# Optimization experiments

Measured on AMD Instinct MI355X. Metric: run time of the kernel, lower is better.

The kernel has to match this reference:

```python
import jax, jax.numpy as jnp
import numpy as np

RES = (64, 128, 256, 512)
CH = (4, 4, 4, 4)          # hidden_dim_voxel
N = 1 << 20                # query points
IN = sum(CH)               # MLP input dim = 16
WIDTH = 64
DEPTH = 4
OUT = 4
A = -0.75                  # torch bicubic coefficient


def setup_inputs() -> dict:
    key = jax.random.key(0)
    ks = jax.random.split(key, 16)
    inp = {"x": jax.random.normal(ks[0], (N, 2), jnp.float32)}
    for i, (r, c) in enumerate(zip(RES, CH)):
        # torch.rand init for voxel data, stored as [C, H, W]
        inp[f"data{i}"] = jax.random.uniform(ks[1 + i], (c, r, r), dtype=jnp.float32)
    dims = [IN] + [WIDTH] * DEPTH
    for i in range(DEPTH):
        fan = dims[i]
        inp[f"w{i}"] = jax.random.normal(ks[5 + i], (fan, WIDTH), jnp.float32) / np.sqrt(fan)
        inp[f"b{i}"] = jnp.zeros((WIDTH,), jnp.float32)
    inp["wout"] = jax.random.normal(ks[9], (WIDTH, OUT), jnp.float32) / np.sqrt(WIDTH)
    inp["bout"] = jnp.zeros((OUT,), jnp.float32)
    return inp


def _cc1(t):  # |x| in [0,1]
    return ((A + 2.0) * t - (A + 3.0)) * t * t + 1.0


def _cc2(t):  # |x| in (1,2]
    return ((A * t - 5.0 * A) * t + 8.0 * A) * t - 4.0 * A


def _cubic_w(t):
    # weights for taps at offsets (-1, 0, 1, 2); t is fractional part, shape [N]
    return jnp.stack([_cc2(t + 1.0), _cc1(t), _cc1(1.0 - t), _cc2(2.0 - t)])  # [4, N]


def _grid_sample_bicubic(data, iy, ix):
    # data: [C, H, W]; iy/ix: unnormalized (align_corners=True) coords, [N]
    # padding_mode='border' -> clamp tap indices
    C, H, W = data.shape
    x0 = jnp.floor(ix)
    y0 = jnp.floor(iy)
    tx = ix - x0
    ty = iy - y0
    offs = jnp.arange(-1, 3, dtype=jnp.int32)[:, None]          # [4,1]
    xs = jnp.clip(x0.astype(jnp.int32)[None] + offs, 0, W - 1)  # [4,N]
    ys = jnp.clip(y0.astype(jnp.int32)[None] + offs, 0, H - 1)  # [4,N]
    wx = _cubic_w(tx)  # [4,N]
    wy = _cubic_w(ty)  # [4,N]
    patch = data[:, ys[:, None, :], xs[None, :, :]]             # [C,4,4,N]
    return jnp.einsum('cijn,in,jn->nc', patch, wy, wx)          # [N,C]


def _forward(x, datas, ws, bs, wout, bout):
    s = jax.nn.sigmoid(x)  # input_activation, enable_act=True
    # Voxel: g = s*2-1, flip(-1); grid_sample align_corners=True unnormalize:
    # (g+1)/2*(size-1) == s*(size-1). After flip, grid x (width) = s[:,1], y = s[:,0].
    feats = []
    for data in datas:
        H = data.shape[1]
        iy = s[:, 0] * (H - 1)
        ix = s[:, 1] * (H - 1)
        feats.append(_grid_sample_bicubic(data, iy, ix))
    h = jnp.concatenate(feats, axis=-1)  # [N, 16]
    inputs = h  # MLP called with enable_act=False
    for i, (w, b) in enumerate(zip(ws, bs)):
        h = jax.nn.relu(h @ w + b)
        if i % 4 == 0 and i > 0:  # skip_layer=4; never triggers for depth=4
            h = jnp.concatenate([h, inputs], axis=-1)
    return h @ wout + bout  # [N, OUT]


def reference(x, data0, data1, data2, data3, w0, b0, w1, b1, w2, b2, w3, b3, wout, bout):
    return _forward(x, (data0, data1, data2, data3), (w0, w1, w2, w3), (b0, b1, b2, b3), wout, bout)
```

## Files before the change

kernel.cpp:

```cpp
#include <hip/hip_runtime.h>

#define A_COEF (-0.75f)

typedef unsigned int u32;
using f16x8 = __attribute__((ext_vector_type(8))) _Float16;
using f32x16 = __attribute__((ext_vector_type(16))) float;

#define NBINS 4096
#define HB    128
#define NBLK  1024

#define ILV_TOTAL  1392640
#define ILV_BLOCKS 5440
#define FRG_BLOCKS 8
#define PREP_BLOCKS (ILV_BLOCKS + FRG_BLOCKS + HB)

__device__ __forceinline__ float cc1(float t) {
    return ((A_COEF + 2.0f) * t - (A_COEF + 3.0f)) * t * t + 1.0f;
}
__device__ __forceinline__ float cc2(float t) {
    return ((A_COEF * t - 5.0f * A_COEF) * t + 8.0f * A_COEF) * t - 4.0f * A_COEF;
}

__device__ __forceinline__ u32 pkrtz(float a, float b) {
    u32 r;
    asm("v_cvt_pkrtz_f16_f32 %0, %1, %2" : "=v"(r) : "v"(a), "v"(b));
    return r;
}

__device__ __forceinline__ int point_bin(float2 xv) {
    float sy = 1.0f / (1.0f + __expf(-xv.x));
    float sx = 1.0f / (1.0f + __expf(-xv.y));
    int qy = min(63, (int)(sy * 64.0f));
    int qx = min(63, (int)(sx * 64.0f));
    return qy * 64 + qx;
}

__global__ __launch_bounds__(256)
void prep_kernel(const float* __restrict__ d0, const float* __restrict__ d1,
                 const float* __restrict__ d2, const float* __restrict__ d3,
                 const float* __restrict__ w0, const float* __restrict__ w1,
                 const float* __restrict__ w2, const float* __restrict__ w3,
                 const float* __restrict__ wout,
                 const float* __restrict__ x, int N, int chunk,
                 float* __restrict__ tab, unsigned short* __restrict__ fr,
                 u32* __restrict__ hist_local) {
    __shared__ u32 lh[NBINS];
    int blk = blockIdx.x;

    if (blk < ILV_BLOCKS) {
        int i = blk * 256 + threadIdx.x;
        if (i >= ILV_TOTAL) return;
        const float* in; int base, RR;
        if (i < 81920) {
            if (i < 16384) { in = d0; base = 0;      RR = 4096;  }
            else           { in = d1; base = 16384;  RR = 16384; }
        } else {
            if (i < 344064){ in = d2; base = 81920;  RR = 65536; }
            else           { in = d3; base = 344064; RR = 262144;}
        }
        int local = i - base;
        tab[i] = in[(local & 3) * RR + (local >> 2)];
        return;
    }

    if (blk < ILV_BLOCKS + FRG_BLOCKS) {
        int t = (blk - ILV_BLOCKS) * 256 + threadIdx.x;
        if (t >= 30 * 64) return;
        int P = t >> 6, lane = t & 63;
        int layer, mt, ks;
        if (P < 2)       { layer = 0; mt = P; ks = 0; }
        else if (P < 26) { int r = P - 2; layer = 1 + r / 8; mt = (r & 7) >> 2; ks = r & 3; }
        else             { layer = 4; mt = 0; ks = P - 26; }

        const float* W; int Mdim, Kdim;
        if (layer == 0)      { W = w0;   Mdim = 64; Kdim = 16; }
        else if (layer == 1) { W = w1;   Mdim = 64; Kdim = 64; }
        else if (layer == 2) { W = w2;   Mdim = 64; Kdim = 64; }
        else if (layer == 3) { W = w3;   Mdim = 64; Kdim = 64; }
        else                 { W = wout; Mdim = 4;  Kdim = 64; }

        int m = mt * 32 + (lane & 31);
        int g = lane >> 5;
        unsigned short o[8];
#pragma unroll
        for (int jj = 0; jj < 8; ++jj) {
            int k = ks * 16 + 8 * (jj >> 2) + 4 * g + (jj & 3);
            float v = (m < Mdim && k < Kdim) ? W[k * Mdim + m] : 0.0f;
            _Float16 h = (_Float16)v;
            o[jj] = *(unsigned short*)&h;
        }
        u32 a = (u32)o[0] | ((u32)o[1] << 16);
        u32 b = (u32)o[2] | ((u32)o[3] << 16);
        u32 c = (u32)o[4] | ((u32)o[5] << 16);
        u32 d = (u32)o[6] | ((u32)o[7] << 16);
        uint4 val; val.x = a; val.y = b; val.z = c; val.w = d;
        *(uint4*)(fr + (size_t)P * 512 + lane * 8) = val;
        return;
    }

    int b = blk - ILV_BLOCKS - FRG_BLOCKS;
    for (int i = threadIdx.x; i < NBINS; i += 256) lh[i] = 0u;
    __syncthreads();
    int start = b * chunk;
    int end = min(start + chunk, N);
    for (int p = start + threadIdx.x; p < end; p += 256) {
        float2 xv = ((const float2*)x)[p];
        atomicAdd(&lh[point_bin(xv)], 1u);
    }
    __syncthreads();
    for (int i = threadIdx.x; i < NBINS; i += 256)
        hist_local[(size_t)b * NBINS + i] = lh[i];
}

__global__ __launch_bounds__(256)
void scanA_kernel(u32* __restrict__ hist_local, u32* __restrict__ tot) {
    int bin = blockIdx.x * 256 + threadIdx.x;
    u32 run = 0;
#pragma unroll 8
    for (int b = 0; b < HB; ++b) {
        u32 v = hist_local[(size_t)b * NBINS + bin];
        hist_local[(size_t)b * NBINS + bin] = run;
        run += v;
    }
    tot[bin] = run;
}

__global__ __launch_bounds__(1024)
void scanB_kernel(const u32* __restrict__ tot, u32* __restrict__ base) {
    __shared__ u32 part[1024];
    int t = threadIdx.x;
    uint4 h = ((const uint4*)tot)[t];
    part[t] = h.x + h.y + h.z + h.w;
    __syncthreads();
    for (int off = 1; off < 1024; off <<= 1) {
        u32 v = (t >= off) ? part[t - off] : 0u;
        __syncthreads();
        part[t] += v;
        __syncthreads();
    }
    u32 excl = (t > 0) ? part[t - 1] : 0u;
    uint4 o;
    o.x = excl; o.y = excl + h.x; o.z = excl + h.x + h.y; o.w = excl + h.x + h.y + h.z;
    ((uint4*)base)[t] = o;
}

__global__ __launch_bounds__(256)
void scatter_kernel(const float* __restrict__ x, int N, int chunk,
                    const u32* __restrict__ hist_local, const u32* __restrict__ base,
                    u32* __restrict__ pidx, float2* __restrict__ sxy) {
    __shared__ u32 off[NBINS];
    int b = blockIdx.x;
    for (int i = threadIdx.x; i < NBINS; i += 256)
        off[i] = base[i] + hist_local[(size_t)b * NBINS + i];
    __syncthreads();
    int start = b * chunk;
    int end = min(start + chunk, N);
    for (int p = start + threadIdx.x; p < end; p += 256) {
        float2 xv = ((const float2*)x)[p];
        int bin = point_bin(xv);
        u32 pos = atomicAdd(&off[bin], 1u);
        float sy = 1.0f / (1.0f + expf(-xv.x));
        float sx = 1.0f / (1.0f + expf(-xv.y));
        pidx[pos] = (u32)p;
        sxy[pos] = make_float2(sy, sx);
    }
}

__device__ __forceinline__ float4 sample_lvl(const float4* __restrict__ tb, int R, float sy, float sx) {
    float RM1f = (float)(R - 1);
    float fy = sy * RM1f, fx = sx * RM1f;
    float y0f = floorf(fy), x0f = floorf(fx);
    float ty = fy - y0f, tx = fx - x0f;
    int y0 = (int)y0f, x0 = (int)x0f;
    float wxa[4] = {cc2(tx + 1.0f), cc1(tx), cc1(1.0f - tx), cc2(2.0f - tx)};
    float wya[4] = {cc2(ty + 1.0f), cc1(ty), cc1(1.0f - ty), cc2(2.0f - ty)};
    int xs[4], ys[4];
#pragma unroll
    for (int j = 0; j < 4; ++j) {
        xs[j] = min(max(x0 - 1 + j, 0), R - 1);
        ys[j] = min(max(y0 - 1 + j, 0), R - 1);
    }
    float a0 = 0.f, a1 = 0.f, a2 = 0.f, a3 = 0.f;
#pragma unroll
    for (int i = 0; i < 4; ++i) {
        const float4* rp = tb + (size_t)ys[i] * R;
        float r0 = 0.f, r1 = 0.f, r2 = 0.f, r3 = 0.f;
#pragma unroll
        for (int j = 0; j < 4; ++j) {
            float4 v = rp[xs[j]];
            r0 = fmaf(wxa[j], v.x, r0);
            r1 = fmaf(wxa[j], v.y, r1);
            r2 = fmaf(wxa[j], v.z, r2);
            r3 = fmaf(wxa[j], v.w, r3);
        }
        a0 = fmaf(wya[i], r0, a0);
        a1 = fmaf(wya[i], r1, a1);
        a2 = fmaf(wya[i], r2, a2);
        a3 = fmaf(wya[i], r3, a3);
    }
    return make_float4(a0, a1, a2, a3);
}

__device__ __forceinline__ f16x8 pack8(const u32 b[4]) {
    union { u32 u[4]; f16x8 v; } t;
    t.u[0] = b[0]; t.u[1] = b[1]; t.u[2] = b[2]; t.u[3] = b[3];
    return t.v;
}

template <int NKS>
__device__ __forceinline__ void mlp_layer(const unsigned short* __restrict__ fl, int pbase, int lane,
                                          const u32 (&B)[4][4],
                                          const float* __restrict__ bias64, f32x16* __restrict__ acc) {
    int g = lane >> 5;
#pragma unroll
    for (int mt = 0; mt < 2; ++mt) {
        f32x16 a;
        const float* bb = bias64 + 4 * g + 32 * mt;
#pragma unroll
        for (int q = 0; q < 4; ++q) {
            float4 b4 = *(const float4*)(bb + 8 * q);
            a[4 * q + 0] = b4.x; a[4 * q + 1] = b4.y; a[4 * q + 2] = b4.z; a[4 * q + 3] = b4.w;
        }
#pragma unroll
        for (int ks = 0; ks < NKS; ++ks) {
            const f16x8 av = *(const f16x8*)(fl + ((size_t)(pbase + mt * NKS + ks)) * 512 + lane * 8);
            a = __builtin_amdgcn_mfma_f32_32x32x16_f16(av, pack8(B[ks]), a, 0, 0, 0);
        }
        acc[mt] = a;
    }
}

__device__ __forceinline__ void acc_to_B(const f32x16* __restrict__ acc, u32 (&B)[4][4]) {
#pragma unroll
    for (int ks = 0; ks < 4; ++ks) {
#pragma unroll
        for (int w = 0; w < 4; ++w) {
            const int r0 = 8 * (ks & 1) + 4 * (w >> 1) + 2 * (w & 1);
            float va = fmaxf(acc[ks >> 1][r0], 0.f);
            float vb = fmaxf(acc[ks >> 1][r0 + 1], 0.f);
            B[ks][w] = pkrtz(va, vb);
        }
    }
}

template <int MODE>
__global__ __launch_bounds__(512, 4)
void mrv_mfma_kernel(const float* __restrict__ x,
                     const float* __restrict__ tex_f,
                     const unsigned short* __restrict__ frg,
                     const u32* __restrict__ pidx,
                     const float2* __restrict__ sxy,
                     const float* __restrict__ b0, const float* __restrict__ b1,
                     const float* __restrict__ b2, const float* __restrict__ b3,
                     const float* __restrict__ bout,
                     float* __restrict__ out, int N, int nbatch, int nper) {
    __shared__ __attribute__((aligned(16))) unsigned short frag_lds[30 * 512];
    __shared__ __attribute__((aligned(16))) float bias_lds[4 * 64];

    {
        const uint4* src = (const uint4*)frg;
        uint4* dst = (uint4*)frag_lds;
#pragma unroll
        for (int i = 0; i < 4; ++i) {
            int idx = threadIdx.x + i * 512;
            if (idx < 1920) dst[idx] = src[idx];
        }
        if (threadIdx.x < 256) {
            int L = threadIdx.x >> 6, i = threadIdx.x & 63;
            const float* bp = (L == 0) ? b0 : (L == 1) ? b1 : (L == 2) ? b2 : b3;
            bias_lds[threadIdx.x] = bp[i];
        }
    }
    __syncthreads();

    const int lane = threadIdx.x & 63;
    const int wid = threadIdx.x >> 6;
    const int g = lane >> 5;
    const float4 bo = *(const float4*)bout;
    const float4* tex = (const float4*)tex_f;

    for (int it = 0; it < nper; ++it) {
        int batch = blockIdx.x * nper + it;
        if (batch >= nbatch) break;
        int slot = batch * 256 + wid * 32 + (lane & 31);
        int sc = min(slot, N - 1);

        int p; float sy, sx;
        if constexpr (MODE == 0) {
            float2 s = sxy[sc];
            sy = s.x; sx = s.y;
            p = (int)pidx[sc];
        } else {
            p = sc;
            float2 xv = ((const float2*)x)[p];
            sy = 1.0f / (1.0f + expf(-xv.x));
            sx = 1.0f / (1.0f + expf(-xv.y));
        }

        float f[8];
#pragma unroll
        for (int lv = 0; lv < 2; ++lv) {
            int lvl = g + 2 * lv;
            int off4 = (lvl == 0) ? 0 : (lvl == 1) ? 4096 : (lvl == 2) ? 20480 : 86016;
            int R = 64 << lvl;
            float4 s = sample_lvl(tex + off4, R, sy, sx);
            f[4 * lv + 0] = s.x; f[4 * lv + 1] = s.y; f[4 * lv + 2] = s.z; f[4 * lv + 3] = s.w;
        }

        u32 B[4][4];
#pragma unroll
        for (int w = 0; w < 4; ++w) B[0][w] = pkrtz(f[2 * w], f[2 * w + 1]);

        f32x16 acc[2];
        mlp_layer<1>(frag_lds, 0,  lane, B, bias_lds + 0,   acc);
        acc_to_B(acc, B);
        mlp_layer<4>(frag_lds, 2,  lane, B, bias_lds + 64,  acc);
        acc_to_B(acc, B);
        mlp_layer<4>(frag_lds, 10, lane, B, bias_lds + 128, acc);
        acc_to_B(acc, B);
        mlp_layer<4>(frag_lds, 18, lane, B, bias_lds + 192, acc);
        acc_to_B(acc, B);

        f32x16 ao;
#pragma unroll
        for (int r = 0; r < 16; ++r)
            ao[r] = (g == 0 && r < 4) ? ((r == 0) ? bo.x : (r == 1) ? bo.y : (r == 2) ? bo.z : bo.w) : 0.0f;
#pragma unroll
        for (int ks = 0; ks < 4; ++ks) {
            const f16x8 av = *(const f16x8*)(frag_lds + ((size_t)(26 + ks)) * 512 + lane * 8);
            ao = __builtin_amdgcn_mfma_f32_32x32x16_f16(av, pack8(B[ks]), ao, 0, 0, 0);
        }
        if (g == 0 && slot < N)
            ((float4*)out)[p] = make_float4(ao[0], ao[1], ao[2], ao[3]);
    }
}

__global__ __launch_bounds__(256)
void mrv_fallback_kernel(const float* __restrict__ x,
                         const float* __restrict__ d0, const float* __restrict__ d1,
                         const float* __restrict__ d2, const float* __restrict__ d3,
                         const float* __restrict__ w0, const float* __restrict__ b0,
                         const float* __restrict__ w1, const float* __restrict__ b1,
                         const float* __restrict__ w2, const float* __restrict__ b2,
                         const float* __restrict__ w3, const float* __restrict__ b3,
                         const float* __restrict__ wout, const float* __restrict__ bout,
                         float* __restrict__ out, int n_pts) {
    int n = blockIdx.x * blockDim.x + threadIdx.x;
    if (n >= n_pts) return;
    const float2 xv = *reinterpret_cast<const float2*>(x + (size_t)2 * n);
    float sy = 1.0f / (1.0f + expf(-xv.x));
    float sx = 1.0f / (1.0f + expf(-xv.y));
    float feats[16];
    const float* ds[4] = {d0, d1, d2, d3};
#pragma unroll
    for (int l = 0; l < 4; ++l) {
        int R = 64 << l;
        float RM1f = (float)(R - 1);
        float fy = sy * RM1f, fx = sx * RM1f;
        float y0f = floorf(fy), x0f = floorf(fx);
        float ty = fy - y0f, tx = fx - x0f;
        int y0 = (int)y0f, x0 = (int)x0f;
        float wxa[4] = {cc2(tx + 1.0f), cc1(tx), cc1(1.0f - tx), cc2(2.0f - tx)};
        float wya[4] = {cc2(ty + 1.0f), cc1(ty), cc1(1.0f - ty), cc2(2.0f - ty)};
        int xs[4], ys[4];
#pragma unroll
        for (int j = 0; j < 4; ++j) {
            xs[j] = min(max(x0 - 1 + j, 0), R - 1);
            ys[j] = min(max(y0 - 1 + j, 0), R - 1);
        }
#pragma unroll
        for (int c = 0; c < 4; ++c) {
            const float* cp = ds[l] + (size_t)c * R * R;
            float ac = 0.f;
#pragma unroll
            for (int i = 0; i < 4; ++i) {
                const float* rowp = cp + (size_t)(ys[i] * R);
                float r = 0.f;
#pragma unroll
                for (int j = 0; j < 4; ++j) r = fmaf(wxa[j], rowp[xs[j]], r);
                ac = fmaf(wya[i], r, ac);
            }
            feats[l * 4 + c] = ac;
        }
    }
    float ha[64], hb[64];
#pragma unroll
    for (int j = 0; j < 64; ++j) ha[j] = b0[j];
#pragma unroll
    for (int k = 0; k < 16; ++k) {
        float fk = feats[k];
#pragma unroll
        for (int j = 0; j < 64; ++j) ha[j] = fmaf(fk, w0[k * 64 + j], ha[j]);
    }
#pragma unroll
    for (int j = 0; j < 64; ++j) ha[j] = fmaxf(ha[j], 0.f);
#define LYR(IN, OUT, W, B)                                                  \
    _Pragma("unroll") for (int j = 0; j < 64; ++j) OUT[j] = (B)[j];         \
    _Pragma("unroll") for (int k = 0; k < 64; ++k) {                        \
        float fk = IN[k];                                                   \
        _Pragma("unroll") for (int j = 0; j < 64; ++j)                      \
            OUT[j] = fmaf(fk, (W)[k * 64 + j], OUT[j]);                     \
    }                                                                       \
    _Pragma("unroll") for (int j = 0; j < 64; ++j) OUT[j] = fmaxf(OUT[j], 0.f);
    LYR(ha, hb, w1, b1)
    LYR(hb, ha, w2, b2)
    LYR(ha, hb, w3, b3)
    float o0 = bout[0], o1 = bout[1], o2 = bout[2], o3 = bout[3];
#pragma unroll
    for (int k = 0; k < 64; ++k) {
        float fk = hb[k];
        o0 = fmaf(fk, wout[k * 4 + 0], o0);
        o1 = fmaf(fk, wout[k * 4 + 1], o1);
        o2 = fmaf(fk, wout[k * 4 + 2], o2);
        o3 = fmaf(fk, wout[k * 4 + 3], o3);
    }
    *reinterpret_cast<float4*>(out + (size_t)n * 4) = make_float4(o0, o1, o2, o3);
}

extern "C" void kernel_launch(void* const* d_in, const int* in_sizes, int n_in,
                              void* d_out, int out_size, void* d_ws, size_t ws_size,
                              hipStream_t stream) {
    const float* x  = (const float*)d_in[0];
    const float* d0 = (const float*)d_in[1];
    const float* d1 = (const float*)d_in[2];
    const float* d2 = (const float*)d_in[3];
    const float* d3 = (const float*)d_in[4];
    const float* w0 = (const float*)d_in[5];
    const float* b0 = (const float*)d_in[6];
    const float* w1 = (const float*)d_in[7];
    const float* b1 = (const float*)d_in[8];
    const float* w2 = (const float*)d_in[9];
    const float* b2 = (const float*)d_in[10];
    const float* w3 = (const float*)d_in[11];
    const float* b3 = (const float*)d_in[12];
    const float* wout = (const float*)d_in[13];
    const float* bout = (const float*)d_in[14];
    float* out = (float*)d_out;

    const int N = in_sizes[0] / 2;

    const size_t ftot = ILV_TOTAL;
    const size_t bytes_tab  = ftot * sizeof(float);
    const size_t bytes_frg  = (size_t)60 * 512 * sizeof(unsigned short);
    const size_t bytes_hist = (size_t)HB * NBINS * sizeof(u32);
    const size_t bytes_tb   = (size_t)NBINS * sizeof(u32) * 2;
    const size_t bytes_sxy  = (size_t)N * sizeof(float2);
    const size_t bytes_pidx = (size_t)N * sizeof(u32);
    const size_t need_mid  = bytes_tab + bytes_frg;
    const size_t need_full = need_mid + bytes_hist + bytes_tb + bytes_sxy + bytes_pidx;

    if (ws_size < need_mid) {
        int blocks = (N + 255) / 256;
        hipLaunchKernelGGL(mrv_fallback_kernel, dim3(blocks), dim3(256), 0, stream,
                           x, d0, d1, d2, d3, w0, b0, w1, b1, w2, b2, w3, b3, wout, bout, out, N);
        return;
    }

    float* ws = (float*)d_ws;
    unsigned short* frg = (unsigned short*)(ws + ftot);
    u32* hist_local = (u32*)((char*)d_ws + need_mid);
    u32* tot  = (u32*)((char*)d_ws + need_mid + bytes_hist);
    u32* base = tot + NBINS;
    float2* sxy = (float2*)((char*)d_ws + need_mid + bytes_hist + bytes_tb);
    u32* pidx = (u32*)((char*)d_ws + need_mid + bytes_hist + bytes_tb + bytes_sxy);

    const int nbatch = (N + 255) / 256;
    const int nper = (nbatch + NBLK - 1) / NBLK;
    const int chunk = (N + HB - 1) / HB;

    if (ws_size >= need_full) {
        hipLaunchKernelGGL(prep_kernel, dim3(PREP_BLOCKS), dim3(256), 0, stream,
                           d0, d1, d2, d3, w0, w1, w2, w3, wout, x, N, chunk,
                           ws, frg, hist_local);
        hipLaunchKernelGGL(scanA_kernel, dim3(NBINS / 256), dim3(256), 0, stream, hist_local, tot);
        hipLaunchKernelGGL(scanB_kernel, dim3(1), dim3(1024), 0, stream, tot, base);
        hipLaunchKernelGGL(scatter_kernel, dim3(HB), dim3(256), 0, stream,
                           x, N, chunk, hist_local, base, pidx, sxy);
        hipLaunchKernelGGL((mrv_mfma_kernel<0>), dim3(NBLK), dim3(512), 0, stream,
                           x, ws, frg, pidx, sxy, b0, b1, b2, b3, bout, out, N, nbatch, nper);
    } else {
        hipLaunchKernelGGL(prep_kernel, dim3(ILV_BLOCKS + FRG_BLOCKS), dim3(256), 0, stream,
                           d0, d1, d2, d3, w0, w1, w2, w3, wout, x, N, chunk,
                           ws, frg, hist_local);
        hipLaunchKernelGGL((mrv_mfma_kernel<2>), dim3(NBLK), dim3(512), 0, stream,
                           x, ws, frg, (const u32*)nullptr, (const float2*)nullptr,
                           b0, b1, b2, b3, bout, out, N, nbatch, nper);
    }
}
```

Before: 126.1 us.

## Process two point batches per iteration and vectorize texture interleave

The main kernel now handles two 256-point sub-batches per loop iteration, issuing both sets of bicubic texture gathers before running the two MLP chains. This is meant to give more memory-level parallelism and hide gather latency behind MFMA work. The prep interleave now writes one float4 per thread instead of scalar stores, cutting the thread count by four. Holding two sets of sampled features live raises register pressure, which could lower occupancy under the 512x4 launch bound.

```diff
diff --git a/kernel.cpp b/kernel.cpp
--- a/kernel.cpp
+++ b/kernel.cpp
@@ -11,7 +11,8 @@
 #define NBLK  1024
 
 #define ILV_TOTAL  1392640
-#define ILV_BLOCKS 5440
+#define ILV_Q      348160
+#define ILV_BLOCKS 1360
 #define FRG_BLOCKS 8
 #define PREP_BLOCKS (ILV_BLOCKS + FRG_BLOCKS + HB)
 
@@ -49,8 +50,9 @@
     int blk = blockIdx.x;
 
     if (blk < ILV_BLOCKS) {
-        int i = blk * 256 + threadIdx.x;
-        if (i >= ILV_TOTAL) return;
+        int q = blk * 256 + threadIdx.x;
+        if (q >= ILV_Q) return;
+        int i = q * 4;
         const float* in; int base, RR;
         if (i < 81920) {
             if (i < 16384) { in = d0; base = 0;      RR = 4096;  }
@@ -59,8 +61,13 @@
             if (i < 344064){ in = d2; base = 81920;  RR = 65536; }
             else           { in = d3; base = 344064; RR = 262144;}
         }
-        int local = i - base;
-        tab[i] = in[(local & 3) * RR + (local >> 2)];
+        int t = (i - base) >> 2;
+        float4 v;
+        v.x = in[0 * RR + t];
+        v.y = in[1 * RR + t];
+        v.z = in[2 * RR + t];
+        v.w = in[3 * RR + t];
+        ((float4*)tab)[q] = v;
         return;
     }
 
@@ -202,6 +209,24 @@
     return make_float4(a0, a1, a2, a3);
 }
 
+__device__ __forceinline__ uint4 sample_B0(const float4* __restrict__ tex, int g, float sy, float sx) {
+    float f[8];
+#pragma unroll
+    for (int lv = 0; lv < 2; ++lv) {
+        int lvl = g + 2 * lv;
+        int off4 = (lvl == 0) ? 0 : (lvl == 1) ? 4096 : (lvl == 2) ? 20480 : 86016;
+        int R = 64 << lvl;
+        float4 s = sample_lvl(tex + off4, R, sy, sx);
+        f[4 * lv + 0] = s.x; f[4 * lv + 1] = s.y; f[4 * lv + 2] = s.z; f[4 * lv + 3] = s.w;
+    }
+    uint4 r;
+    r.x = pkrtz(f[0], f[1]);
+    r.y = pkrtz(f[2], f[3]);
+    r.z = pkrtz(f[4], f[5]);
+    r.w = pkrtz(f[6], f[7]);
+    return r;
+}
+
 __device__ __forceinline__ f16x8 pack8(const u32 b[4]) {
     union { u32 u[4]; f16x8 v; } t;
     t.u[0] = b[0]; t.u[1] = b[1]; t.u[2] = b[2]; t.u[3] = b[3];
@@ -242,6 +267,37 @@
             B[ks][w] = pkrtz(va, vb);
         }
     }
+}
+
+__device__ __forceinline__ void mlp_and_store(const unsigned short* __restrict__ frag_lds,
+                                              const float* __restrict__ bias_lds,
+                                              int lane, int g, const float4& bo,
+                                              u32 b00, u32 b01, u32 b02, u32 b03,
+                                              float* __restrict__ out, int p, bool valid) {
+    u32 B[4][4];
+    B[0][0] = b00; B[0][1] = b01; B[0][2] = b02; B[0][3] = b03;
+
+    f32x16 acc[2];
+    mlp_layer<1>(frag_lds, 0,  lane, B, bias_lds + 0,   acc);
+    acc_to_B(acc, B);
+    mlp_layer<4>(frag_lds, 2,  lane, B, bias_lds + 64,  acc);
+    acc_to_B(acc, B);
+    mlp_layer<4>(frag_lds, 10, lane, B, bias_lds + 128, acc);
+    acc_to_B(acc, B);
+    mlp_layer<4>(frag_lds, 18, lane, B, bias_lds + 192, acc);
+    acc_to_B(acc, B);
+
+    f32x16 ao;
+#pragma unroll
+    for (int r = 0; r < 16; ++r)
+        ao[r] = (g == 0 && r < 4) ? ((r == 0) ? bo.x : (r == 1) ? bo.y : (r == 2) ? bo.z : bo.w) : 0.0f;
+#pragma unroll
+    for (int ks = 0; ks < 4; ++ks) {
+        const f16x8 av = *(const f16x8*)(frag_lds + ((size_t)(26 + ks)) * 512 + lane * 8);
+        ao = __builtin_amdgcn_mfma_f32_32x32x16_f16(av, pack8(B[ks]), ao, 0, 0, 0);
+    }
+    if (g == 0 && valid)
+        ((float4*)out)[p] = make_float4(ao[0], ao[1], ao[2], ao[3]);
 }
 
 template <int MODE>
@@ -283,56 +339,34 @@
     for (int it = 0; it < nper; ++it) {
         int batch = blockIdx.x * nper + it;
         if (batch >= nbatch) break;
-        int slot = batch * 256 + wid * 32 + (lane & 31);
-        int sc = min(slot, N - 1);
-
-        int p; float sy, sx;
+        int slotA = batch * 512 + wid * 32 + (lane & 31);
+        int slotB = slotA + 256;
+        int scA = min(slotA, N - 1);
+        int scB = min(slotB, N - 1);
+
+        int pA, pB; float syA, sxA, syB, sxB;
         if constexpr (MODE == 0) {
-            float2 s = sxy[sc];
-            sy = s.x; sx = s.y;
-            p = (int)pidx[sc];
+            float2 sA = sxy[scA];
+            float2 sB = sxy[scB];
+            syA = sA.x; sxA = sA.y;
+            syB = sB.x; sxB = sB.y;
+            pA = (int)pidx[scA];
+            pB = (int)pidx[scB];
         } else {
-            p = sc;
-            float2 xv = ((const float2*)x)[p];
-            sy = 1.0f / (1.0f + expf(-xv.x));
-            sx = 1.0f / (1.0f + expf(-xv.y));
-        }
-
-        float f[8];
-#pragma unroll
-        for (int lv = 0; lv < 2; ++lv) {
-            int lvl = g + 2 * lv;
-            int off4 = (lvl == 0) ? 0 : (lvl == 1) ? 4096 : (lvl == 2) ? 20480 : 86016;
-            int R = 64 << lvl;
-            float4 s = sample_lvl(tex + off4, R, sy, sx);
-            f[4 * lv + 0] = s.x; f[4 * lv + 1] = s.y; f[4 * lv + 2] = s.z; f[4 * lv + 3] = s.w;
-        }
-
-        u32 B[4][4];
-#pragma unroll
-        for (int w = 0; w < 4; ++w) B[0][w] = pkrtz(f[2 * w], f[2 * w + 1]);
-
-        f32x16 acc[2];
-        mlp_layer<1>(frag_lds, 0,  lane, B, bias_lds + 0,   acc);
-        acc_to_B(acc, B);
-        mlp_layer<4>(frag_lds, 2,  lane, B, bias_lds + 64,  acc);
-        acc_to_B(acc, B);
-        mlp_layer<4>(frag_lds, 10, lane, B, bias_lds + 128, acc);
-        acc_to_B(acc, B);
-        mlp_layer<4>(frag_lds, 18, lane, B, bias_lds + 192, acc);
-        acc_to_B(acc, B);
-
-        f32x16 ao;
-#pragma unroll
-        for (int r = 0; r < 16; ++r)
-            ao[r] = (g == 0 && r < 4) ? ((r == 0) ? bo.x : (r == 1) ? bo.y : (r == 2) ? bo.z : bo.w) : 0.0f;
-#pragma unroll
-        for (int ks = 0; ks < 4; ++ks) {
-            const f16x8 av = *(const f16x8*)(frag_lds + ((size_t)(26 + ks)) * 512 + lane * 8);
-            ao = __builtin_amdgcn_mfma_f32_32x32x16_f16(av, pack8(B[ks]), ao, 0, 0, 0);
-        }
-        if (g == 0 && slot < N)
-            ((float4*)out)[p] = make_float4(ao[0], ao[1], ao[2], ao[3]);
+            pA = scA; pB = scB;
+            float2 xvA = ((const float2*)x)[pA];
+            float2 xvB = ((const float2*)x)[pB];
+            syA = 1.0f / (1.0f + expf(-xvA.x));
+            sxA = 1.0f / (1.0f + expf(-xvA.y));
+            syB = 1.0f / (1.0f + expf(-xvB.x));
+            sxB = 1.0f / (1.0f + expf(-xvB.y));
+        }
+
+        uint4 a0 = sample_B0(tex, g, syA, sxA);
+        uint4 bb0 = sample_B0(tex, g, syB, sxB);
+
+        mlp_and_store(frag_lds, bias_lds, lane, g, bo, a0.x, a0.y, a0.z, a0.w, out, pA, slotA < N);
+        mlp_and_store(frag_lds, bias_lds, lane, g, bo, bb0.x, bb0.y, bb0.z, bb0.w, out, pB, slotB < N);
     }
 }
 
@@ -465,7 +499,7 @@
     float2* sxy = (float2*)((char*)d_ws + need_mid + bytes_hist + bytes_tb);
     u32* pidx = (u32*)((char*)d_ws + need_mid + bytes_hist + bytes_tb + bytes_sxy);
 
-    const int nbatch = (N + 255) / 256;
+    const int nbatch = (N + 511) / 512;
     const int nper = (nbatch + NBLK - 1) / NBLK;
     const int chunk = (N + HB - 1) / HB;
 
```

New measurement: 501.0 us. 3.97x slower.
